# Performance work log

Hardware: AMD Instinct MI355X
Metric: run time of the kernel (lower is better)

## Reference

```python
import jax, jax.numpy as jnp
import numpy as np

IN_F, OUT_F = 1024, 1024
GRID_SIZE, SPLINE_ORDER = 5, 3
BATCH = 4096
GRID_LO, GRID_HI = -1.0, 1.0


def _make_grid():
    h = (GRID_HI - GRID_LO) / GRID_SIZE
    g = jnp.arange(-SPLINE_ORDER, GRID_SIZE + SPLINE_ORDER + 1, dtype=jnp.float32) * h + GRID_LO  # [12]
    return jnp.broadcast_to(g, (IN_F, g.shape[0]))  # [in, 12]


def setup_inputs() -> dict:
    key = jax.random.key(0)
    k1, k2, k3 = jax.random.split(key, 3)
    x = jax.random.normal(k1, (BATCH, IN_F), dtype=jnp.float32)
    base_weight = jax.random.normal(k2, (OUT_F, IN_F), dtype=jnp.float32) * (1.0 / np.sqrt(IN_F))
    spline_weight = jax.random.normal(k3, (OUT_F, IN_F, GRID_SIZE + SPLINE_ORDER), dtype=jnp.float32) * 0.1
    spline_scaler = jnp.ones((OUT_F, IN_F), dtype=jnp.float32)
    grid = _make_grid()
    return {"x": x, "base_weight": base_weight, "spline_weight": spline_weight,
            "spline_scaler": spline_scaler, "grid": grid}


def b_splines(x, grid):
    # x: [B, in], grid: [in, 12] -> bases: [B, in, grid_size+spline_order]
    xe = x[..., None]  # [B, in, 1]
    bases = ((xe >= grid[:, :-1]) & (xe < grid[:, 1:])).astype(x.dtype)  # [B, in, 11]
    for k in range(1, SPLINE_ORDER + 1):
        t0 = grid[:, :-(k + 1)]
        t1 = grid[:, k:-1]
        t2 = grid[:, k + 1:]
        t3 = grid[:, 1:-k]
        bases = ((xe - t0) / (t1 - t0 + 1e-8) * bases[..., :-1]
                 + (t2 - xe) / (t2 - t3 + 1e-8) * bases[..., 1:])
    return bases


def reference(x, base_weight, spline_weight, spline_scaler, grid):
    base_output = jax.nn.silu(x) @ base_weight.T  # [B, out]
    spline_basis = b_splines(x, grid)             # [B, in, 8]
    spline_output = jnp.einsum('bij,oij,oi->bo', spline_basis, spline_weight, spline_scaler)
    return base_output + spline_output
```

## Files before the change

### kernel.cpp

```cpp
#include <hip/hip_runtime.h>
#include <hip/hip_bf16.h>
#include <stdint.h>
#include <stddef.h>

#define IN_F     1024
#define OUT_F    1024
#define BATCH    4096
#define NSPLINE  8
#define KDIM     (IN_F * 9)
#define GRIDPTS  12

typedef __bf16 bf16;
typedef __bf16 bf16x8 __attribute__((ext_vector_type(8)));
typedef float  f32x4  __attribute__((ext_vector_type(4)));

#define NB_BUILD (BATCH * IN_F / 256)
#define NB_PACK  (OUT_F * IN_F / 256)

__global__ __launch_bounds__(256) void prep(const float* __restrict__ x,
                                            const float* __restrict__ grid,
                                            const float* __restrict__ bw,
                                            const float* __restrict__ sw,
                                            const float* __restrict__ sc,
                                            bf16* __restrict__ A,
                                            bf16* __restrict__ W)
{
    __shared__ float g[GRIDPTS];
    __shared__ float rec[33];

    if (blockIdx.x < NB_BUILD) {
        if (threadIdx.x < GRIDPTS) g[threadIdx.x] = grid[threadIdx.x];
        __syncthreads();
        if (threadIdx.x < 33) {
            const int k = threadIdx.x / 11 + 1;
            const int j = threadIdx.x % 11;
            if (j + k <= 11) rec[threadIdx.x] = 1.0f / (g[j + k] - g[j] + 1e-8f);
        }
        __syncthreads();

        const int idx = blockIdx.x * 256 + threadIdx.x;
        const int b = idx >> 10;
        const int i = idx & 1023;
        const float xv = x[idx];

        float bs[11];
#pragma unroll
        for (int j = 0; j < 11; ++j)
            bs[j] = (xv >= g[j] && xv < g[j + 1]) ? 1.0f : 0.0f;

#pragma unroll
        for (int k = 1; k <= 3; ++k) {
            const float* rk = &rec[(k - 1) * 11];
#pragma unroll
            for (int j = 0; j < 10; ++j) {
                if (j <= 10 - k) {
                    bs[j] = (xv - g[j]) * rk[j] * bs[j]
                          + (g[j + k + 1] - xv) * rk[j + 1] * bs[j + 1];
                }
            }
        }

        const float si = xv / (1.0f + __expf(-xv));

        bf16* rowp = A + (size_t)b * KDIM;
        rowp[i] = (bf16)si;
#pragma unroll
        for (int j = 0; j < NSPLINE; ++j)
            rowp[(size_t)(j + 1) * IN_F + i] = (bf16)bs[j];
    } else {
        const int idx = (blockIdx.x - NB_BUILD) * 256 + threadIdx.x;
        const int i = idx & 1023;
        const float s = sc[idx];

        bf16* rowp = W + (size_t)(idx >> 10) * KDIM;
        rowp[i] = (bf16)bw[idx];

        const float4* swv = (const float4*)(sw + (size_t)idx * NSPLINE);
        const float4 w0 = swv[0];
        const float4 w1 = swv[1];
        rowp[(size_t)1 * IN_F + i] = (bf16)(w0.x * s);
        rowp[(size_t)2 * IN_F + i] = (bf16)(w0.y * s);
        rowp[(size_t)3 * IN_F + i] = (bf16)(w0.z * s);
        rowp[(size_t)4 * IN_F + i] = (bf16)(w0.w * s);
        rowp[(size_t)5 * IN_F + i] = (bf16)(w1.x * s);
        rowp[(size_t)6 * IN_F + i] = (bf16)(w1.y * s);
        rowp[(size_t)7 * IN_F + i] = (bf16)(w1.z * s);
        rowp[(size_t)8 * IN_F + i] = (bf16)(w1.w * s);
    }
}

#define BM8 256
#define BN8 256
#define BK8 64
#define SPLIT 4

#define GLOAD_LDS16(gp, lp)                                                          \
    __builtin_amdgcn_global_load_lds((const __attribute__((address_space(1))) void*)(gp), \
                                     (__attribute__((address_space(3))) void*)(lp), 16, 0, 0)

__global__ __launch_bounds__(512, 2) void gemm8(const bf16* __restrict__ A,
                                                const bf16* __restrict__ B,
                                                float* __restrict__ C,
                                                int kLen)
{
    __shared__ bf16 lds[8 * 8192];

    const int tid  = threadIdx.x;
    const int wave = tid >> 6;
    const int lane = tid & 63;

    const int nwg  = gridDim.x;
    const int q    = nwg >> 3;
    const int wgid = (blockIdx.x & 7) * q + (blockIdx.x >> 3);
    const int nxy  = (BATCH / BM8) * (OUT_F / BN8);
    const int z    = wgid / nxy;
    const int rem  = wgid - z * nxy;
    const int by   = rem >> 4;
    const int bx   = rem & 15;

    const int bm   = bx * BM8;
    const int bcol = by * BN8;
    const int kBase = z * kLen;
    C += (size_t)z * BATCH * OUT_F;

    const int wr = (wave >> 2) * 128;
    const int wc = (wave & 3) * 64;

    f32x4 acc[8][4] = {};

    const int NT   = kLen / BK8;
    const int hmax = 4 * NT;

    const int srow = tid >> 2;
    const int sch  = (((tid & 3) ^ ((tid >> 3) & 3))) * 8;
    const bf16* baseA = A + (size_t)(bm + srow) * KDIM + kBase + sch;
    const bf16* baseB = B + (size_t)(bcol + srow) * KDIM + kBase + sch;
    const size_t rstep = (size_t)128 * KDIM;
    bf16* ldsw = &lds[wave * 512];

    auto stage = [&](int h) {
        if (h < hmax) {
            const int t   = h >> 2;
            const int th  = h & 3;
            const int kof = t * BK8 + ((th >> 1) ? 32 : 0);
            const bf16* src = (th & 1) ? baseB : baseA;
            bf16* l0 = ldsw + (h & 7) * 8192;
            GLOAD_LDS16(src + kof, l0);
            GLOAD_LDS16(src + kof + rstep, l0 + 4096);
        }
    };

    for (int h = 0; h < 6; ++h) stage(h);
    asm volatile("s_waitcnt vmcnt(4)" ::: "memory");
    __builtin_amdgcn_s_barrier();

    const int rowk = lane & 15;
    const int kc   = lane >> 4;
    const int kxor = (kc ^ ((rowk >> 1) & 3)) * 8;

#define LDSFRAG(slot, row) (*(const bf16x8*)&lds[(slot) * 8192 + (row) * 32 + kxor])

    bf16x8 a[4], b[4], a2[4], b2[4];
#pragma unroll
    for (int m = 0; m < 4; ++m) a[m] = LDSFRAG(0, wr + m * 16 + rowk);
#pragma unroll
    for (int n = 0; n < 4; ++n) b[n] = LDSFRAG(1, wc + n * 16 + rowk);

    for (int t = 0; t < NT; ++t) {
        const int h0  = 4 * t;
        const int sA0 = (h0 + 0) & 7;
        const int sA1 = (h0 + 2) & 7, sB1 = (h0 + 3) & 7;

        stage(h0 + 6);
#pragma unroll
        for (int m = 0; m < 4; ++m) a2[m] = LDSFRAG(sA0, wr + 64 + m * 16 + rowk);
        __builtin_amdgcn_sched_barrier(0);
        __builtin_amdgcn_s_setprio(1);
#pragma unroll
        for (int m = 0; m < 4; ++m)
#pragma unroll
            for (int n = 0; n < 4; ++n)
                acc[m][n] = __builtin_amdgcn_mfma_f32_16x16x32_bf16(a[m], b[n], acc[m][n], 0, 0, 0);
        __builtin_amdgcn_s_setprio(0);
        __builtin_amdgcn_s_barrier();

        stage(h0 + 7);
#pragma unroll
        for (int m = 0; m < 4; ++m) a[m] = LDSFRAG(sA1, wr + m * 16 + rowk);
#pragma unroll
        for (int n = 0; n < 4; ++n) b2[n] = LDSFRAG(sB1, wc + n * 16 + rowk);
        __builtin_amdgcn_sched_barrier(0);
        __builtin_amdgcn_s_setprio(1);
#pragma unroll
        for (int m = 0; m < 4; ++m)
#pragma unroll
            for (int n = 0; n < 4; ++n)
                acc[4 + m][n] = __builtin_amdgcn_mfma_f32_16x16x32_bf16(a2[m], b[n], acc[4 + m][n], 0, 0, 0);
        __builtin_amdgcn_s_setprio(0);
        __builtin_amdgcn_s_barrier();

        stage(h0 + 8);
#pragma unroll
        for (int m = 0; m < 4; ++m) a2[m] = LDSFRAG(sA1, wr + 64 + m * 16 + rowk);
        __builtin_amdgcn_sched_barrier(0);
        __builtin_amdgcn_s_setprio(1);
#pragma unroll
        for (int m = 0; m < 4; ++m)
#pragma unroll
            for (int n = 0; n < 4; ++n)
                acc[m][n] = __builtin_amdgcn_mfma_f32_16x16x32_bf16(a[m], b2[n], acc[m][n], 0, 0, 0);
        __builtin_amdgcn_s_setprio(0);
        __builtin_amdgcn_s_barrier();

        stage(h0 + 9);
        __builtin_amdgcn_sched_barrier(0);
        __builtin_amdgcn_s_setprio(1);
#pragma unroll
        for (int m = 0; m < 4; ++m)
#pragma unroll
            for (int n = 0; n < 4; ++n)
                acc[4 + m][n] = __builtin_amdgcn_mfma_f32_16x16x32_bf16(a2[m], b2[n], acc[4 + m][n], 0, 0, 0);
        __builtin_amdgcn_s_setprio(0);
        if (t < NT - 2)       asm volatile("s_waitcnt vmcnt(4)" ::: "memory");
        else if (t == NT - 2) asm volatile("s_waitcnt vmcnt(0)" ::: "memory");
        if (t + 1 < NT) {
            const int nA0 = (h0 + 4) & 7, nB0 = (h0 + 5) & 7;
#pragma unroll
            for (int m = 0; m < 4; ++m) a[m] = LDSFRAG(nA0, wr + m * 16 + rowk);
#pragma unroll
            for (int n = 0; n < 4; ++n) b[n] = LDSFRAG(nB0, wc + n * 16 + rowk);
        }
        __builtin_amdgcn_s_barrier();
    }
#undef LDSFRAG

    const int ccol = lane & 15;
    const int crow = (lane >> 4) * 4;
#pragma unroll
    for (int mf = 0; mf < 8; ++mf) {
#pragma unroll
        for (int nf = 0; nf < 4; ++nf) {
            float* cp = C + (size_t)(bm + wr + mf * 16 + crow) * OUT_F + (bcol + wc + nf * 16 + ccol);
#pragma unroll
            for (int r = 0; r < 4; ++r)
                cp[(size_t)r * OUT_F] = acc[mf][nf][r];
        }
    }
}

__global__ __launch_bounds__(256) void reduce_partials(const float4* __restrict__ P,
                                                       float4* __restrict__ out,
                                                       int n4)
{
    const int stride = gridDim.x * 256;
    for (int i = blockIdx.x * 256 + threadIdx.x; i < n4; i += stride) {
        float4 s = P[i];
#pragma unroll
        for (int p = 1; p < SPLIT; ++p) {
            const float4 q = P[(size_t)p * n4 + i];
            s.x += q.x; s.y += q.y; s.z += q.z; s.w += q.w;
        }
        out[i] = s;
    }
}

extern "C" void kernel_launch(void* const* d_in, const int* in_sizes, int n_in,
                              void* d_out, int out_size, void* d_ws, size_t ws_size,
                              hipStream_t stream)
{
    const float* x  = (const float*)d_in[0];
    const float* bw = (const float*)d_in[1];
    const float* sw = (const float*)d_in[2];
    const float* sc = (const float*)d_in[3];
    const float* gr = (const float*)d_in[4];
    float* out = (float*)d_out;

    bf16* A = (bf16*)d_ws;
    bf16* W = A + (size_t)BATCH * KDIM;
    float* parts = (float*)(W + (size_t)OUT_F * KDIM);

    prep<<<NB_BUILD + NB_PACK, 256, 0, stream>>>(x, gr, bw, sw, sc, A, W);

    const int nblk = (BATCH / BM8) * (OUT_F / BN8) * SPLIT;
    gemm8<<<nblk, 512, 0, stream>>>(A, W, parts, KDIM / SPLIT);

    const int n4 = BATCH * OUT_F / 4;
    reduce_partials<<<2048, 256, 0, stream>>>((const float4*)parts, (float4*)out, n4);
}
```

Before: 121.6 us.

## Load B fragments directly from global into registers, staging only A in LDS

The B operand no longer goes through LDS. Each wave loads its own B fragments straight from global memory into a register double buffer (bcur/bnxt), prefetching one K-tile ahead. Only A is staged through the LDS ring, and the per-tile loop drops from four workgroup barriers to one. The aim is to cut LDS traffic and barrier stalls, at the cost of many more VGPRs, duplicate global B reads across the two wave rows, vmcnt waits that now also cover the B loads, and a loop that assumes an even number of tiles.

Result: slower. 250.9 us (+106.3%).

```diff
diff --git a/kernel.cpp b/kernel.cpp
--- a/kernel.cpp
+++ b/kernel.cpp
@@ -128,110 +128,103 @@
 
     f32x4 acc[8][4] = {};
 
-    const int NT   = kLen / BK8;
-    const int hmax = 4 * NT;
+    const int NT = kLen / BK8;
+    const int hA = 2 * NT;
 
     const int srow = tid >> 2;
     const int sch  = (((tid & 3) ^ ((tid >> 3) & 3))) * 8;
     const bf16* baseA = A + (size_t)(bm + srow) * KDIM + kBase + sch;
-    const bf16* baseB = B + (size_t)(bcol + srow) * KDIM + kBase + sch;
     const size_t rstep = (size_t)128 * KDIM;
     bf16* ldsw = &lds[wave * 512];
 
-    auto stage = [&](int h) {
-        if (h < hmax) {
-            const int t   = h >> 2;
-            const int th  = h & 3;
-            const int kof = t * BK8 + ((th >> 1) ? 32 : 0);
-            const bf16* src = (th & 1) ? baseB : baseA;
+    auto stageA = [&](int h) {
+        if (h < hA) {
+            const int kof = (h >> 1) * BK8 + (h & 1) * 32;
             bf16* l0 = ldsw + (h & 7) * 8192;
-            GLOAD_LDS16(src + kof, l0);
-            GLOAD_LDS16(src + kof + rstep, l0 + 4096);
+            GLOAD_LDS16(baseA + kof, l0);
+            GLOAD_LDS16(baseA + kof + rstep, l0 + 4096);
         }
     };
-
-    for (int h = 0; h < 6; ++h) stage(h);
-    asm volatile("s_waitcnt vmcnt(4)" ::: "memory");
-    __builtin_amdgcn_s_barrier();
 
     const int rowk = lane & 15;
     const int kc   = lane >> 4;
     const int kxor = (kc ^ ((rowk >> 1) & 3)) * 8;
 
+    const bf16* bp = B + (size_t)(bcol + wc + rowk) * KDIM + kBase + kc * 8;
+
+    bf16x8 bcur[8], bnxt[8];
+
+#pragma unroll
+    for (int kh = 0; kh < 2; ++kh)
+#pragma unroll
+        for (int n = 0; n < 4; ++n)
+            bcur[kh * 4 + n] = *(const bf16x8*)(bp + (size_t)(n * 16) * KDIM + kh * 32);
+    for (int h = 0; h < 6; ++h) stageA(h);
+    asm volatile("s_waitcnt vmcnt(4)" ::: "memory");
+    __builtin_amdgcn_s_barrier();
+
 #define LDSFRAG(slot, row) (*(const bf16x8*)&lds[(slot) * 8192 + (row) * 32 + kxor])
 
-    bf16x8 a[4], b[4], a2[4], b2[4];
+    bf16x8 a[4], a2[4];
 #pragma unroll
     for (int m = 0; m < 4; ++m) a[m] = LDSFRAG(0, wr + m * 16 + rowk);
-#pragma unroll
-    for (int n = 0; n < 4; ++n) b[n] = LDSFRAG(1, wc + n * 16 + rowk);
-
-    for (int t = 0; t < NT; ++t) {
-        const int h0  = 4 * t;
-        const int sA0 = (h0 + 0) & 7;
-        const int sA1 = (h0 + 2) & 7, sB1 = (h0 + 3) & 7;
-
-        stage(h0 + 6);
-#pragma unroll
-        for (int m = 0; m < 4; ++m) a2[m] = LDSFRAG(sA0, wr + 64 + m * 16 + rowk);
-        __builtin_amdgcn_sched_barrier(0);
-        __builtin_amdgcn_s_setprio(1);
-#pragma unroll
-        for (int m = 0; m < 4; ++m)
-#pragma unroll
-            for (int n = 0; n < 4; ++n)
-                acc[m][n] = __builtin_amdgcn_mfma_f32_16x16x32_bf16(a[m], b[n], acc[m][n], 0, 0, 0);
-        __builtin_amdgcn_s_setprio(0);
-        __builtin_amdgcn_s_barrier();
-
-        stage(h0 + 7);
-#pragma unroll
-        for (int m = 0; m < 4; ++m) a[m] = LDSFRAG(sA1, wr + m * 16 + rowk);
-#pragma unroll
-        for (int n = 0; n < 4; ++n) b2[n] = LDSFRAG(sB1, wc + n * 16 + rowk);
-        __builtin_amdgcn_sched_barrier(0);
-        __builtin_amdgcn_s_setprio(1);
-#pragma unroll
-        for (int m = 0; m < 4; ++m)
-#pragma unroll
-            for (int n = 0; n < 4; ++n)
-                acc[4 + m][n] = __builtin_amdgcn_mfma_f32_16x16x32_bf16(a2[m], b[n], acc[4 + m][n], 0, 0, 0);
-        __builtin_amdgcn_s_setprio(0);
-        __builtin_amdgcn_s_barrier();
-
-        stage(h0 + 8);
-#pragma unroll
-        for (int m = 0; m < 4; ++m) a2[m] = LDSFRAG(sA1, wr + 64 + m * 16 + rowk);
-        __builtin_amdgcn_sched_barrier(0);
-        __builtin_amdgcn_s_setprio(1);
-#pragma unroll
-        for (int m = 0; m < 4; ++m)
-#pragma unroll
-            for (int n = 0; n < 4; ++n)
-                acc[m][n] = __builtin_amdgcn_mfma_f32_16x16x32_bf16(a[m], b2[n], acc[m][n], 0, 0, 0);
-        __builtin_amdgcn_s_setprio(0);
-        __builtin_amdgcn_s_barrier();
-
-        stage(h0 + 9);
-        __builtin_amdgcn_sched_barrier(0);
-        __builtin_amdgcn_s_setprio(1);
-#pragma unroll
-        for (int m = 0; m < 4; ++m)
-#pragma unroll
-            for (int n = 0; n < 4; ++n)
-                acc[4 + m][n] = __builtin_amdgcn_mfma_f32_16x16x32_bf16(a2[m], b2[n], acc[4 + m][n], 0, 0, 0);
-        __builtin_amdgcn_s_setprio(0);
-        if (t < NT - 2)       asm volatile("s_waitcnt vmcnt(4)" ::: "memory");
-        else if (t == NT - 2) asm volatile("s_waitcnt vmcnt(0)" ::: "memory");
-        if (t + 1 < NT) {
-            const int nA0 = (h0 + 4) & 7, nB0 = (h0 + 5) & 7;
-#pragma unroll
-            for (int m = 0; m < 4; ++m) a[m] = LDSFRAG(nA0, wr + m * 16 + rowk);
-#pragma unroll
-            for (int n = 0; n < 4; ++n) b[n] = LDSFRAG(nB0, wc + n * 16 + rowk);
-        }
-        __builtin_amdgcn_s_barrier();
-    }
+
+#define TILE(T, BC, BN_)                                                              \
+  { const int t_ = (T);                                                               \
+    const int s0 = (2 * t_) & 7, s1 = (2 * t_ + 1) & 7, s2 = (2 * t_ + 2) & 7;        \
+    if (t_ + 1 < NT) {                                                                \
+      _Pragma("unroll") for (int kh = 0; kh < 2; ++kh)                                \
+      _Pragma("unroll") for (int n = 0; n < 4; ++n)                                   \
+        BN_[kh * 4 + n] = *(const bf16x8*)(bp + (size_t)(n * 16) * KDIM               \
+                                           + (t_ + 1) * BK8 + kh * 32);               \
+    }                                                                                 \
+    __builtin_amdgcn_sched_barrier(0);                                                \
+                          \
+    stageA(2 * t_ + 6);                                                               \
+    _Pragma("unroll") for (int m = 0; m < 4; ++m) a2[m] = LDSFRAG(s0, wr + 64 + m * 16 + rowk); \
+    __builtin_amdgcn_sched_barrier(0);                                                \
+    __builtin_amdgcn_s_setprio(1);                                                    \
+    _Pragma("unroll") for (int m = 0; m < 4; ++m)                                     \
+    _Pragma("unroll") for (int n = 0; n < 4; ++n)                                     \
+      acc[m][n] = __builtin_amdgcn_mfma_f32_16x16x32_bf16(a[m], BC[n], acc[m][n], 0, 0, 0); \
+    __builtin_amdgcn_s_setprio(0);                                                    \
+                                  \
+    _Pragma("unroll") for (int m = 0; m < 4; ++m) a[m] = LDSFRAG(s1, wr + m * 16 + rowk); \
+    __builtin_amdgcn_sched_barrier(0);                                                \
+    __builtin_amdgcn_s_setprio(1);                                                    \
+    _Pragma("unroll") for (int m = 0; m < 4; ++m)                                     \
+    _Pragma("unroll") for (int n = 0; n < 4; ++n)                                     \
+      acc[4 + m][n] = __builtin_amdgcn_mfma_f32_16x16x32_bf16(a2[m], BC[n], acc[4 + m][n], 0, 0, 0); \
+    __builtin_amdgcn_s_setprio(0);                                                    \
+                                  \
+    stageA(2 * t_ + 7);                                                               \
+    _Pragma("unroll") for (int m = 0; m < 4; ++m) a2[m] = LDSFRAG(s1, wr + 64 + m * 16 + rowk); \
+    __builtin_amdgcn_sched_barrier(0);                                                \
+    __builtin_amdgcn_s_setprio(1);                                                    \
+    _Pragma("unroll") for (int m = 0; m < 4; ++m)                                     \
+    _Pragma("unroll") for (int n = 0; n < 4; ++n)                                     \
+      acc[m][n] = __builtin_amdgcn_mfma_f32_16x16x32_bf16(a[m], BC[4 + n], acc[m][n], 0, 0, 0); \
+    __builtin_amdgcn_s_setprio(0);                                                    \
+     \
+    if (t_ < NT - 2)       asm volatile("s_waitcnt vmcnt(4)" ::: "memory");           \
+    else if (t_ == NT - 2) asm volatile("s_waitcnt vmcnt(0)" ::: "memory");           \
+    if (t_ + 1 < NT) {                                                                \
+      _Pragma("unroll") for (int m = 0; m < 4; ++m) a[m] = LDSFRAG(s2, wr + m * 16 + rowk); \
+    }                                                                                 \
+    __builtin_amdgcn_sched_barrier(0);                                                \
+    __builtin_amdgcn_s_setprio(1);                                                    \
+    _Pragma("unroll") for (int m = 0; m < 4; ++m)                                     \
+    _Pragma("unroll") for (int n = 0; n < 4; ++n)                                     \
+      acc[4 + m][n] = __builtin_amdgcn_mfma_f32_16x16x32_bf16(a2[m], BC[4 + n], acc[4 + m][n], 0, 0, 0); \
+    __builtin_amdgcn_s_setprio(0);                                                    \
+    __builtin_amdgcn_s_barrier();                                                     \
+  }
+
+    for (int tt = 0; tt < NT; tt += 2) {
+        TILE(tt,     bcur, bnxt)
+        TILE(tt + 1, bnxt, bcur)
+    }
+#undef TILE
 #undef LDSFRAG
 
     const int ccol = lane & 15;
```
